# Kernel optimization log

Measured on AMD Instinct MI355X. Metric: run time of the kernel, lower is better.

## Reference

```python
import jax, jax.numpy as jnp
import numpy as np

B, T, D, V, MEM = 2, 512, 512, 256, 256


def _gru(x, h0, wih, whh, bih, bhh):
    # x: [B,T,D], h0: [B,D]; torch GRU gate order: r, z, n
    def step(h, xt):
        gi = xt @ wih.T + bih            # [B,3D]
        gh = h @ whh.T + bhh             # [B,3D]
        i_r, i_z, i_n = jnp.split(gi, 3, axis=-1)
        h_r, h_z, h_n = jnp.split(gh, 3, axis=-1)
        r = jax.nn.sigmoid(i_r + h_r)
        z = jax.nn.sigmoid(i_z + h_z)
        n = jnp.tanh(i_n + r * h_n)
        h_new = (1.0 - z) * n + z * h
        return h_new, h_new
    hT, ys = jax.lax.scan(step, h0, jnp.swapaxes(x, 0, 1))
    return jnp.swapaxes(ys, 0, 1), hT


def _layernorm(x, g, b, eps=1e-5):
    m = jnp.mean(x, axis=-1, keepdims=True)
    v = jnp.mean((x - m) ** 2, axis=-1, keepdims=True)
    return (x - m) / jnp.sqrt(v + eps) * g + b


def setup_inputs() -> dict:
    key = jax.random.key(0)
    ks = jax.random.split(key, 24)
    s = 1.0 / np.sqrt(D)
    inp = {
        'x': jax.random.randint(ks[0], (B, T), 0, V, dtype=jnp.int32),
        'h_f': jnp.zeros((1, B, D), jnp.float32),
        'h_s': jnp.zeros((1, B, D), jnp.float32),
        'soma_w': jax.random.normal(ks[1], (V, D), jnp.float32),
        'fast_wih': jax.random.normal(ks[2], (3 * D, D)) * s,
        'fast_whh': jax.random.normal(ks[3], (3 * D, D)) * s,
        'fast_bih': jax.random.normal(ks[4], (3 * D,)) * s,
        'fast_bhh': jax.random.normal(ks[5], (3 * D,)) * s,
        'slow_wih': jax.random.normal(ks[6], (3 * D, D)) * s,
        'slow_whh': jax.random.normal(ks[7], (3 * D, D)) * s,
        'slow_bih': jax.random.normal(ks[8], (3 * D,)) * s,
        'slow_bhh': jax.random.normal(ks[9], (3 * D,)) * s,
        'qkv_w': jax.random.normal(ks[10], (3 * D, D)) * s,
        'qkv_b': jax.random.normal(ks[11], (3 * D,)) * s,
        'gate_w': jax.random.normal(ks[12], (D, D)) * s,
        'gate_b': jax.random.normal(ks[13], (D,)) * s,
        'gate_g': jnp.ones((D,), jnp.float32),
        'gate_bb': jnp.zeros((D,), jnp.float32),
        'mem_bank': jax.random.normal(ks[14], (MEM, D)) * 0.1,
        'hip_qw': jax.random.normal(ks[15], (D, D)) * s,
        'hip_qb': jax.random.normal(ks[16], (D,)) * s,
        'axon_w': jax.random.normal(ks[17], (D, 4 * D)) * (0.5 * s),
        'axon_b': jax.random.normal(ks[18], (D,)) * s,
        'norm_g': jnp.ones((D,), jnp.float32),
        'norm_b': jnp.zeros((D,), jnp.float32),
    }
    return inp


def reference(x, h_f, h_s, soma_w, fast_wih, fast_whh, fast_bih, fast_bhh,
              slow_wih, slow_whh, slow_bih, slow_bhh, qkv_w, qkv_b,
              gate_w, gate_b, gate_g, gate_bb, mem_bank, hip_qw, hip_qb,
              axon_w, axon_b, norm_g, norm_b):
    d = soma_w.shape[1]
    s_in = soma_w[x]  # mod[0] == 1.0
    p_f, hf1 = _gru(s_in, h_f[0], fast_wih, fast_whh, fast_bih, fast_bhh)
    p_s, hs1 = _gru(p_f, h_s[0], slow_wih, slow_whh, slow_bih, slow_bhh)
    # LinearIntentMemory: naive cumulative outer-product linear attention
    qkv = p_s @ qkv_w.T + qkv_b
    q, k, v = jnp.split(qkv, 3, axis=-1)
    q = jax.nn.elu(q) + 1.0
    k = jax.nn.elu(k) + 1.0
    kv_cum = jnp.cumsum(jnp.einsum('bti,btj->btij', k, v), axis=1)  # [B,T,D,D]
    num = jnp.einsum('bti,btij->btj', q, kv_cum)
    den = jnp.einsum('bti,bti->bt', q, jnp.cumsum(k, axis=1))[..., None] + 1e-6
    l_mem = num / den
    # intent gate: Linear -> LayerNorm -> Tanh
    intent = jnp.tanh(_layernorm(p_s @ gate_w.T + gate_b, gate_g, gate_bb))
    # hippocampus: softmax attention over memory bank
    qh = p_s @ hip_qw.T + hip_qb
    attn = qh @ mem_bank.T / jnp.sqrt(jnp.float32(d))
    episodes = jax.nn.softmax(attn, axis=-1) @ mem_bank
    combined = jnp.concatenate([p_f, intent, l_mem, episodes], axis=-1)
    thought = _layernorm(jnp.tanh(combined @ axon_w.T + axon_b), norm_g, norm_b)
    sw = soma_w / jnp.maximum(jnp.linalg.norm(soma_w, axis=-1, keepdims=True), 1e-12)
    logits = (thought @ sw.T) * 16.0
    return (logits, thought, hf1[None], hs1[None])
```

## Files before the change

kernel.cpp:

```cpp
#include <hip/hip_runtime.h>
#include <cstddef>

#define F_ELUQK 1
#define F_CAUSAL 2
#define F_DIV 4
#define F_NN 8
#define F_SCALE 16
#define F_ROWSUM 32
#define FLAG_STRIDE 4
#define L_WGS 64
#define UNITS 8

enum : int {
  OFF_QH = 0,
  OFF_COMB = 524288,
  OFF_PS = OFF_COMB + 2097152,
  OFF_QKV = OFF_PS + 524288,
  OFF_SCORES = OFF_QKV + 1572864,
  OFF_DEN = OFF_SCORES + 524288,
  OFF_TMP = OFF_DEN + 1024,
  OFF_ATTN = OFF_TMP + 524288,
  OFF_SWN = OFF_ATTN + 262144,
  OFF_RING = OFF_SWN + 256,
  OFF_HSB = OFF_RING + 8192,
  OFF_FLAGS = OFF_HSB + 4096
};

#define BAR() __asm__ __volatile__("s_waitcnt lgkmcnt(0)\n\ts_barrier" ::: "memory")

__global__ __launch_bounds__(256) void gemm(
    const float* __restrict__ A, int lda, const float* __restrict__ B, int ldb,
    float* __restrict__ C, int ldc, int coff, int K,
    const float* __restrict__ bias, const float* __restrict__ den,
    const float* __restrict__ cscale, float* __restrict__ rsum,
    float scale, int flags, int bBatch,
    float* __restrict__ Cz, int kzoff) {
  __shared__ float As[16 * 65];
  __shared__ float Bs[16 * 65];
  int tid = threadIdx.x;
  int n0 = blockIdx.x * 64, m0 = blockIdx.y * 64;
  if (blockIdx.z) { A += kzoff; B += kzoff; C = Cz; bias = nullptr; }
  int rowoff = (m0 >> 9) * bBatch;
  int tx = tid & 15, ty = tid >> 4;

  if ((flags & F_CAUSAL) && n0 > ((m0 & 511) + 63)) {
    #pragma unroll
    for (int i = 0; i < 4; ++i)
      #pragma unroll
      for (int j = 0; j < 4; ++j)
        C[(size_t)(m0 + ty * 4 + i) * ldc + coff + n0 + tx * 4 + j] = 0.f;
    return;
  }

  float acc[4][4] = {};
  for (int k0 = 0; k0 < K; k0 += 16) {
    {
      int rr = tid >> 2, c4 = (tid & 3) << 2;
      const float* ap = A + (size_t)(m0 + rr) * lda + (k0 + c4);
      float4 av = *(const float4*)ap;
      As[(c4 + 0) * 65 + rr] = av.x;
      As[(c4 + 1) * 65 + rr] = av.y;
      As[(c4 + 2) * 65 + rr] = av.z;
      As[(c4 + 3) * 65 + rr] = av.w;
    }
    if (!(flags & F_NN)) {
      int rr = tid >> 2, c4 = (tid & 3) << 2;
      const float* bp = B + (size_t)(n0 + rr + rowoff) * ldb + (k0 + c4);
      float4 bv = *(const float4*)bp;
      Bs[(c4 + 0) * 65 + rr] = bv.x; Bs[(c4 + 1) * 65 + rr] = bv.y;
      Bs[(c4 + 2) * 65 + rr] = bv.z; Bs[(c4 + 3) * 65 + rr] = bv.w;
    } else {
      int kk = tid >> 4, n4 = (tid & 15) << 2;
      const float* bp = B + (size_t)(k0 + kk + rowoff) * ldb + (n0 + n4);
      float4 bv = *(const float4*)bp;
      Bs[kk * 65 + n4 + 0] = bv.x; Bs[kk * 65 + n4 + 1] = bv.y;
      Bs[kk * 65 + n4 + 2] = bv.z; Bs[kk * 65 + n4 + 3] = bv.w;
    }
    __syncthreads();
    #pragma unroll
    for (int k = 0; k < 16; ++k) {
      float av[4], bv[4];
      #pragma unroll
      for (int i = 0; i < 4; ++i) av[i] = As[k * 65 + ty * 4 + i];
      #pragma unroll
      for (int j = 0; j < 4; ++j) bv[j] = Bs[k * 65 + tx * 4 + j];
      #pragma unroll
      for (int i = 0; i < 4; ++i)
        #pragma unroll
        for (int j = 0; j < 4; ++j)
          acc[i][j] = fmaf(av[i], bv[j], acc[i][j]);
    }
    __syncthreads();
  }
  float rs[4] = {0.f, 0.f, 0.f, 0.f};
  #pragma unroll
  for (int i = 0; i < 4; ++i) {
    int m = m0 + ty * 4 + i;
    float dv = (flags & F_DIV) ? (1.0f / (den[m] + 1e-6f)) : 1.0f;
    #pragma unroll
    for (int j = 0; j < 4; ++j) {
      int n = n0 + tx * 4 + j;
      float v = acc[i][j];
      if (bias) v += bias[n];
      if (flags & F_ELUQK) { if (n < 1024) v = (v > 0.f) ? (v + 1.f) : __expf(v); }
      if (flags & F_CAUSAL) { if (n > (m & 511)) v = 0.f; }
      if (flags & F_SCALE) v *= scale;
      if (cscale) v *= cscale[coff + n];
      if (flags & F_DIV) v *= dv;
      C[(size_t)m * ldc + coff + n] = v;
      if (flags & F_ROWSUM) rs[i] += v;
    }
  }
  if (flags & F_ROWSUM) {
    #pragma unroll
    for (int i = 0; i < 4; ++i) {
      float s = rs[i];
      s += __shfl_xor(s, 1); s += __shfl_xor(s, 2);
      s += __shfl_xor(s, 4); s += __shfl_xor(s, 8);
      if (tx == 0) atomicAdd(rsum + (m0 + ty * 4 + i), s);
    }
  }
}

__global__ __launch_bounds__(256) void gemm3(
    const float* __restrict__ A,
    const float* __restrict__ qkvw, const float* __restrict__ qkvb,
    const float* __restrict__ gatew, const float* __restrict__ gateb,
    const float* __restrict__ hipw, const float* __restrict__ hipb,
    float* __restrict__ QKV, float* __restrict__ TMP, float* __restrict__ QH) {
  __shared__ float As[16 * 65];
  __shared__ float Bs[16 * 65];
  int tid = threadIdx.x;
  int n0 = blockIdx.x * 64, m0 = blockIdx.y * 64;
  const float* B; const float* bias; float* C; int ldc, base;
  if (n0 < 1536) { B = qkvw; bias = qkvb; C = QKV; ldc = 1536; base = 0; }
  else if (n0 < 2048) { B = gatew; bias = gateb; C = TMP; ldc = 512; base = 1536; }
  else { B = hipw; bias = hipb; C = QH; ldc = 512; base = 2048; }
  int tx = tid & 15, ty = tid >> 4;
  float acc[4][4] = {};
  for (int k0 = 0; k0 < 512; k0 += 16) {
    {
      int rr = tid >> 2, c4 = (tid & 3) << 2;
      const float* ap = A + (size_t)(m0 + rr) * 512 + (k0 + c4);
      float4 av = *(const float4*)ap;
      As[(c4 + 0) * 65 + rr] = av.x; As[(c4 + 1) * 65 + rr] = av.y;
      As[(c4 + 2) * 65 + rr] = av.z; As[(c4 + 3) * 65 + rr] = av.w;
    }
    {
      int rr = tid >> 2, c4 = (tid & 3) << 2;
      const float* bp = B + (size_t)(n0 - base + rr) * 512 + (k0 + c4);
      float4 bv = *(const float4*)bp;
      Bs[(c4 + 0) * 65 + rr] = bv.x; Bs[(c4 + 1) * 65 + rr] = bv.y;
      Bs[(c4 + 2) * 65 + rr] = bv.z; Bs[(c4 + 3) * 65 + rr] = bv.w;
    }
    __syncthreads();
    #pragma unroll
    for (int k = 0; k < 16; ++k) {
      float av[4], bv[4];
      #pragma unroll
      for (int i = 0; i < 4; ++i) av[i] = As[k * 65 + ty * 4 + i];
      #pragma unroll
      for (int j = 0; j < 4; ++j) bv[j] = Bs[k * 65 + tx * 4 + j];
      #pragma unroll
      for (int i = 0; i < 4; ++i)
        #pragma unroll
        for (int j = 0; j < 4; ++j)
          acc[i][j] = fmaf(av[i], bv[j], acc[i][j]);
    }
    __syncthreads();
  }
  #pragma unroll
  for (int i = 0; i < 4; ++i) {
    int m = m0 + ty * 4 + i;
    #pragma unroll
    for (int j = 0; j < 4; ++j) {
      int n = n0 + tx * 4 + j;
      float v = acc[i][j] + bias[n - base];
      if (n < 1024) v = (v > 0.f) ? (v + 1.f) : __expf(v);
      C[(size_t)m * ldc + (n - base)] = v;
    }
  }
}

__device__ __forceinline__ void post_flag(unsigned* flags, int w, unsigned v) {
  __hip_atomic_store(flags + (size_t)w * FLAG_STRIDE, v, __ATOMIC_RELAXED,
                     __HIP_MEMORY_SCOPE_AGENT);
}
__device__ __forceinline__ void poll64(const unsigned* flags, unsigned tgt, int lane) {
  const unsigned* p = flags + (size_t)lane * FLAG_STRIDE;
  while (__hip_atomic_load(p, __ATOMIC_RELAXED, __HIP_MEMORY_SCOPE_AGENT) < tgt)
    __builtin_amdgcn_s_sleep(1);
}
__device__ __forceinline__ void stage_pull(const unsigned long long* __restrict__ src,
                                           const unsigned* __restrict__ flags,
                                           unsigned tgt, int lane,
                                           float* __restrict__ dstLds) {
  unsigned long long v[16];
  #pragma unroll
  for (int k = 0; k < 16; ++k)
    v[k] = __hip_atomic_load(src + k * 64 + lane, __ATOMIC_RELAXED,
                             __HIP_MEMORY_SCOPE_AGENT);
  unsigned bad = 0;
  #pragma unroll
  for (int k = 0; k < 16; ++k) bad |= ((unsigned)(v[k] >> 32)) ^ tgt;
  if (!__all(bad == 0)) {
    poll64(flags, tgt, lane);
    for (;;) {
      #pragma unroll
      for (int k = 0; k < 16; ++k)
        v[k] = __hip_atomic_load(src + k * 64 + lane, __ATOMIC_RELAXED,
                                 __HIP_MEMORY_SCOPE_AGENT);
      bad = 0;
      #pragma unroll
      for (int k = 0; k < 16; ++k) bad |= ((unsigned)(v[k] >> 32)) ^ tgt;
      if (__all(bad == 0)) break;
      __builtin_amdgcn_s_sleep(1);
    }
  }
  #pragma unroll
  for (int k = 0; k < 16; ++k)
    dstLds[k * 64 + lane] = __uint_as_float((unsigned)v[k]);
}

__global__ __launch_bounds__(256, 1) void gru2_kernel(
    const float* __restrict__ soma, const int* __restrict__ x,
    const float* __restrict__ fwih, const float* __restrict__ fbih,
    const float* __restrict__ fwhh, const float* __restrict__ fbhh,
    const float* __restrict__ h0f,
    const float* __restrict__ swih, const float* __restrict__ sbih,
    const float* __restrict__ swhh, const float* __restrict__ sbhh,
    const float* __restrict__ h0s,
    float* __restrict__ pf_out,
    float* __restrict__ ps_out,
    float* __restrict__ hfT, float* __restrict__ hsT,
    unsigned long long* __restrict__ ringq,
    unsigned long long* __restrict__ hsq,
    unsigned* __restrict__ flagsA, unsigned* __restrict__ flagsB) {
  __shared__ __attribute__((aligned(16))) float hl[1024];
  __shared__ __attribute__((aligned(16))) float inb[2048];
  __shared__ float P[48];
  __shared__ float Q[48];
  __shared__ float bl[24];
  __shared__ float bi[24];
  __shared__ int xl[1024];
  int tid = threadIdx.x, wg = blockIdx.x;
  bool L1 = wg < L_WGS;
  int j0 = (wg & (L_WGS - 1)) * UNITS;
  int part = tid & 7, r = tid >> 3;
  int g = r >> 3, u = r & 7;
  int wave = tid >> 6, lane = tid & 63;
  const float* whh = L1 ? fwhh : swhh;
  const float* bhh = L1 ? fbhh : sbhh;
  const float* wih = L1 ? fwih : swih;
  const float* bih = L1 ? fbih : sbih;

  float4 wh[16], wi[16];
  if (r < 24) {
    const float* wp = whh + (size_t)(g * 512 + j0 + u) * 512 + part * 4;
    #pragma unroll
    for (int i = 0; i < 16; ++i) wh[i] = *(const float4*)(wp + i * 32);
    const float* wp2 = wih + (size_t)(g * 512 + j0 + u) * 512 + part * 4;
    #pragma unroll
    for (int i = 0; i < 16; ++i) wi[i] = *(const float4*)(wp2 + i * 32);
  }
  if (tid < 24) {
    bl[tid] = bhh[(tid >> 3) * 512 + j0 + (tid & 7)];
    bi[tid] = bih[(tid >> 3) * 512 + j0 + (tid & 7)];
  }
  if (L1) {
    for (int q = tid; q < 1024; q += 256) xl[q] = x[q];
  }
  __syncthreads();

  if (wave == 3) {
    if (L1) {
      int r0 = xl[0], r1 = xl[512];
      const float4* sp0 = (const float4*)(soma + (size_t)r0 * 512);
      const float4* sp1 = (const float4*)(soma + (size_t)r1 * 512);
      float4* dst = (float4*)inb;
      dst[lane * 2] = sp0[lane * 2]; dst[lane * 2 + 1] = sp0[lane * 2 + 1];
      dst[128 + lane * 2] = sp1[lane * 2]; dst[128 + lane * 2 + 1] = sp1[lane * 2 + 1];
    } else {
      stage_pull(ringq, flagsA, 1u, lane, inb);
    }
  }
  BAR();

  const float4* h4 = (const float4*)hl;

  if (L1) {
    for (int t = 0; t < 512; ++t) {
      float c0 = 0.f, c1 = 0.f;
      if (wave == 3) {
        if (t == 0) {
          #pragma unroll
          for (int k = 0; k < 16; ++k) hl[k * 64 + lane] = h0f[k * 64 + lane];
          int r0 = xl[1], r1 = xl[513];
          const float4* sp0 = (const float4*)(soma + (size_t)r0 * 512);
          const float4* sp1 = (const float4*)(soma + (size_t)r1 * 512);
          float4* dst = (float4*)(inb + 1024);
          dst[lane * 2] = sp0[lane * 2]; dst[lane * 2 + 1] = sp0[lane * 2 + 1];
          dst[128 + lane * 2] = sp1[lane * 2]; dst[128 + lane * 2 + 1] = sp1[lane * 2 + 1];
        } else {
          if (t + 1 < 512) {
            int r0 = xl[t + 1], r1 = xl[512 + t + 1];
            const float4* sp0 = (const float4*)(soma + (size_t)r0 * 512);
            const float4* sp1 = (const float4*)(soma + (size_t)r1 * 512);
            float4* dst = (float4*)(inb + ((t + 1) & 1) * 1024);
            dst[lane * 2] = sp0[lane * 2]; dst[lane * 2 + 1] = sp0[lane * 2 + 1];
            dst[128 + lane * 2] = sp1[lane * 2];
            dst[128 + lane * 2 + 1] = sp1[lane * 2 + 1];
            __builtin_amdgcn_sched_barrier(0);
          }
          stage_pull(ringq + (size_t)((t - 1) & 3) * 1024, flagsA,
                     (unsigned)t, lane, hl);
        }
      } else {
        const float4* f4v = (const float4*)(inb + (t & 1) * 1024);
        #pragma unroll
        for (int i = 0; i < 16; ++i) {
          float4 v = wi[i];
          float4 y0 = f4v[i * 8 + part];
          float4 y1 = f4v[128 + i * 8 + part];
          c0 += v.x * y0.x + v.y * y0.y + v.z * y0.z + v.w * y0.w;
          c1 += v.x * y1.x + v.y * y1.y + v.z * y1.z + v.w * y1.w;
        }
      }
      BAR();
      if (wave != 3) {
        float a0 = 0.f, a1 = 0.f;
        #pragma unroll
        for (int i = 0; i < 16; ++i) {
          float4 w = wh[i];
          float4 x0 = h4[i * 8 + part];
          float4 x1 = h4[128 + i * 8 + part];
          a0 += w.x * x0.x + w.y * x0.y + w.z * x0.z + w.w * x0.w;
          a1 += w.x * x1.x + w.y * x1.y + w.z * x1.z + w.w * x1.w;
        }
        a0 += __shfl_xor(a0, 1); a0 += __shfl_xor(a0, 2); a0 += __shfl_xor(a0, 4);
        a1 += __shfl_xor(a1, 1); a1 += __shfl_xor(a1, 2); a1 += __shfl_xor(a1, 4);
        c0 += __shfl_xor(c0, 1); c0 += __shfl_xor(c0, 2); c0 += __shfl_xor(c0, 4);
        c1 += __shfl_xor(c1, 1); c1 += __shfl_xor(c1, 2); c1 += __shfl_xor(c1, 4);
        if (part == 0) { P[r] = a0; P[24 + r] = a1; Q[r] = c0; Q[24 + r] = c1; }
      } else {
        if (t >= 4) poll64(flagsB, (unsigned)(t - 3), lane);
      }
      BAR();
      if (wave == 3 && lane < 16) {
        int b = lane >> 3, u2 = lane & 7, j = j0 + u2;
        float i_r = Q[b * 24 + u2] + bi[u2];
        float i_z = Q[b * 24 + 8 + u2] + bi[8 + u2];
        float i_n = Q[b * 24 + 16 + u2] + bi[16 + u2];
        float gh_r = P[b * 24 + u2] + bl[u2];
        float gh_z = P[b * 24 + 8 + u2] + bl[8 + u2];
        float gh_n = P[b * 24 + 16 + u2] + bl[16 + u2];
        float hold = hl[b * 512 + j];
        float rg = 1.0f / (1.0f + __expf(-(i_r + gh_r)));
        float zg = 1.0f / (1.0f + __expf(-(i_z + gh_z)));
        float ng = tanhf(i_n + rg * gh_n);
        float hnew = (1.0f - zg) * ng + zg * hold;
        unsigned long long pv =
            ((unsigned long long)(unsigned)(t + 1) << 32) |
            (unsigned long long)__float_as_uint(hnew);
        __hip_atomic_store(ringq + (size_t)(t & 3) * 1024 + b * 512 + j, pv,
                           __ATOMIC_RELAXED, __HIP_MEMORY_SCOPE_AGENT);
        if (lane == 0) post_flag(flagsA, wg, (unsigned)(t + 1));
        pf_out[(size_t)(b * 512 + t) * 2048 + j] = hnew;
        if (t == 511) hfT[b * 512 + j] = hnew;
      }
    }
  } else {
    for (int t2 = 0; t2 < 512; ++t2) {
      float c0 = 0.f, c1 = 0.f;
      if (wave == 3) {
        if (t2 == 0) {
          #pragma unroll
          for (int k = 0; k < 16; ++k) hl[k * 64 + lane] = h0s[k * 64 + lane];
        }
        if (t2 + 1 < 512) {
          stage_pull(ringq + (size_t)((t2 + 1) & 3) * 1024, flagsA,
                     (unsigned)(t2 + 2), lane, inb + ((t2 + 1) & 1) * 1024);
          __builtin_amdgcn_sched_barrier(0);
        }
        if (t2 > 0) {
          stage_pull(hsq + (size_t)((t2 - 1) & 1) * 1024, flagsB,
                     (unsigned)t2, lane, hl);
        }
      } else {
        const float4* f4v = (const float4*)(inb + (t2 & 1) * 1024);
        #pragma unroll
        for (int i = 0; i < 16; ++i) {
          float4 v = wi[i];
          float4 y0 = f4v[i * 8 + part];
          float4 y1 = f4v[128 + i * 8 + part];
          c0 += v.x * y0.x + v.y * y0.y + v.z * y0.z + v.w * y0.w;
          c1 += v.x * y1.x + v.y * y1.y + v.z * y1.z + v.w * y1.w;
        }
      }
      BAR();
      if (wave != 3) {
        float a0 = 0.f, a1 = 0.f;
        #pragma unroll
        for (int i = 0; i < 16; ++i) {
          float4 w = wh[i];
          float4 x0 = h4[i * 8 + part];
          float4 x1 = h4[128 + i * 8 + part];
          a0 += w.x * x0.x + w.y * x0.y + w.z * x0.z + w.w * x0.w;
          a1 += w.x * x1.x + w.y * x1.y + w.z * x1.z + w.w * x1.w;
        }
        a0 += __shfl_xor(a0, 1); a0 += __shfl_xor(a0, 2); a0 += __shfl_xor(a0, 4);
        a1 += __shfl_xor(a1, 1); a1 += __shfl_xor(a1, 2); a1 += __shfl_xor(a1, 4);
        c0 += __shfl_xor(c0, 1); c0 += __shfl_xor(c0, 2); c0 += __shfl_xor(c0, 4);
        c1 += __shfl_xor(c1, 1); c1 += __shfl_xor(c1, 2); c1 += __shfl_xor(c1, 4);
        if (part == 0) { P[r] = a0; P[24 + r] = a1; Q[r] = c0; Q[24 + r] = c1; }
      }
      BAR();
      if (wave == 3 && lane < 16) {
        int b = lane >> 3, u2 = lane & 7, j = j0 + u2;
        float i_r = Q[b * 24 + u2] + bi[u2];
        float i_z = Q[b * 24 + 8 + u2] + bi[8 + u2];
        float i_n = Q[b * 24 + 16 + u2] + bi[16 + u2];
        float gh_r = P[b * 24 + u2] + bl[u2];
        float gh_z = P[b * 24 + 8 + u2] + bl[8 + u2];
        float gh_n = P[b * 24 + 16 + u2] + bl[16 + u2];
        float hold = hl[b * 512 + j];
        float rg = 1.0f / (1.0f + __expf(-(i_r + gh_r)));
        float zg = 1.0f / (1.0f + __expf(-(i_z + gh_z)));
        float ng = tanhf(i_n + rg * gh_n);
        float hnew = (1.0f - zg) * ng + zg * hold;
        unsigned long long pv =
            ((unsigned long long)(unsigned)(t2 + 1) << 32) |
            (unsigned long long)__float_as_uint(hnew);
        __hip_atomic_store(hsq + (size_t)(t2 & 1) * 1024 + b * 512 + j, pv,
                           __ATOMIC_RELAXED, __HIP_MEMORY_SCOPE_AGENT);
        if (lane == 0) post_flag(flagsB, wg - L_WGS, (unsigned)(t2 + 1));
        ps_out[(size_t)(b * 512 + t2) * 512 + j] = hnew;
        if (t2 == 511) hsT[b * 512 + j] = hnew;
      }
    }
  }
}

__global__ __launch_bounds__(256) void softmax_kernel(float* __restrict__ a) {
  int m = blockIdx.x, tid = threadIdx.x;
  float v = a[(size_t)m * 256 + tid];
  float mx = v;
  #pragma unroll
  for (int off = 32; off > 0; off >>= 1) mx = fmaxf(mx, __shfl_down(mx, off));
  __shared__ float r4[4];
  __shared__ float s4[4];
  if ((tid & 63) == 0) r4[tid >> 6] = mx;
  __syncthreads();
  mx = fmaxf(fmaxf(r4[0], r4[1]), fmaxf(r4[2], r4[3]));
  float e = __expf(v - mx);
  float s = e;
  #pragma unroll
  for (int off = 32; off > 0; off >>= 1) s += __shfl_down(s, off);
  if ((tid & 63) == 0) s4[tid >> 6] = s;
  __syncthreads();
  s = s4[0] + s4[1] + s4[2] + s4[3];
  a[(size_t)m * 256 + tid] = e / s;
}

__global__ __launch_bounds__(256) void ln_kernel(
    const float* __restrict__ src, const float* __restrict__ src2,
    float* __restrict__ dst, int ldd, int dcoff,
    const float* __restrict__ gv, const float* __restrict__ bv, int tanhFirst) {
  int m = blockIdx.x, tid = threadIdx.x;
  float x0 = src[(size_t)m * 512 + tid];
  float x1 = src[(size_t)m * 512 + 256 + tid];
  if (src2) { x0 += src2[(size_t)m * 512 + tid]; x1 += src2[(size_t)m * 512 + 256 + tid]; }
  if (tanhFirst) { x0 = tanhf(x0); x1 = tanhf(x1); }
  float s = x0 + x1, ss = x0 * x0 + x1 * x1;
  #pragma unroll
  for (int off = 32; off > 0; off >>= 1) { s += __shfl_down(s, off); ss += __shfl_down(ss, off); }
  __shared__ float rs[4], rss[4];
  if ((tid & 63) == 0) { rs[tid >> 6] = s; rss[tid >> 6] = ss; }
  __syncthreads();
  float st = rs[0] + rs[1] + rs[2] + rs[3];
  float sst = rss[0] + rss[1] + rss[2] + rss[3];
  float mean = st * (1.0f / 512.0f);
  float var = sst * (1.0f / 512.0f) - mean * mean;
  float inv = rsqrtf(var + 1e-5f);
  float y0 = (x0 - mean) * inv * gv[tid] + bv[tid];
  float y1 = (x1 - mean) * inv * gv[256 + tid] + bv[256 + tid];
  if (!tanhFirst) { y0 = tanhf(y0); y1 = tanhf(y1); }
  dst[(size_t)m * ldd + dcoff + tid] = y0;
  dst[(size_t)m * ldd + dcoff + 256 + tid] = y1;
}

__global__ __launch_bounds__(256) void swinv_kernel(const float* __restrict__ soma,
                                                    float* __restrict__ swn) {
  int r = blockIdx.x, tid = threadIdx.x;
  float x0 = soma[(size_t)r * 512 + tid];
  float x1 = soma[(size_t)r * 512 + 256 + tid];
  float ss = x0 * x0 + x1 * x1;
  #pragma unroll
  for (int off = 32; off > 0; off >>= 1) ss += __shfl_down(ss, off);
  __shared__ float r4[4];
  if ((tid & 63) == 0) r4[tid >> 6] = ss;
  __syncthreads();
  if (tid == 0) {
    float norm = fmaxf(sqrtf(r4[0] + r4[1] + r4[2] + r4[3]), 1e-12f);
    swn[r] = 16.0f / norm;
  }
}

extern "C" void kernel_launch(void* const* d_in, const int* in_sizes, int n_in,
                              void* d_out, int out_size, void* d_ws, size_t ws_size,
                              hipStream_t stream) {
  (void)in_sizes; (void)n_in; (void)out_size; (void)ws_size;
  float* W = (float*)d_ws;
  float* outf = (float*)d_out;
  const int* x = (const int*)d_in[0];
  const float* soma = (const float*)d_in[3];

  hipMemsetAsync((char*)d_ws + (size_t)OFF_RING * 4, 0, 51200, stream);
  hipMemsetAsync((char*)d_ws + (size_t)OFF_DEN * 4, 0, 4096, stream);

  gru2_kernel<<<2 * L_WGS, 256, 0, stream>>>(soma, x,
      (const float*)d_in[4], (const float*)d_in[6],
      (const float*)d_in[5], (const float*)d_in[7], (const float*)d_in[1],
      (const float*)d_in[8], (const float*)d_in[10],
      (const float*)d_in[9], (const float*)d_in[11], (const float*)d_in[2],
      W + OFF_COMB, W + OFF_PS, outf + 786432, outf + 787456,
      (unsigned long long*)(W + OFF_RING), (unsigned long long*)(W + OFF_HSB),
      (unsigned*)(W + OFF_FLAGS),
      (unsigned*)(W + OFF_FLAGS) + L_WGS * FLAG_STRIDE);

  gemm3<<<dim3(40, 16), 256, 0, stream>>>(W + OFF_PS,
      (const float*)d_in[12], (const float*)d_in[13],
      (const float*)d_in[14], (const float*)d_in[15],
      (const float*)d_in[19], (const float*)d_in[20],
      W + OFF_QKV, W + OFF_TMP, W + OFF_QH);

  gemm<<<dim3(8, 16), 256, 0, stream>>>(W + OFF_QKV, 1536, W + OFF_QKV + 512, 1536,
      W + OFF_SCORES, 512, 0, 512, nullptr, nullptr, nullptr, W + OFF_DEN,
      1.f, F_CAUSAL | F_ROWSUM, 512, nullptr, 0);

  gemm<<<dim3(8, 16), 256, 0, stream>>>(W + OFF_SCORES, 512, W + OFF_QKV + 1024, 1536,
      W + OFF_COMB, 2048, 1024, 512, nullptr, W + OFF_DEN, nullptr, nullptr,
      1.f, F_NN | F_DIV, 512, nullptr, 0);

  ln_kernel<<<1024, 256, 0, stream>>>(W + OFF_TMP, nullptr, W + OFF_COMB, 2048, 512,
      (const float*)d_in[16], (const float*)d_in[17], 0);

  gemm<<<dim3(4, 16), 256, 0, stream>>>(W + OFF_QH, 512, (const float*)d_in[18], 512,
      W + OFF_ATTN, 256, 0, 512, nullptr, nullptr, nullptr, nullptr,
      0.04419417382415922f, F_SCALE, 0, nullptr, 0);
  softmax_kernel<<<1024, 256, 0, stream>>>(W + OFF_ATTN);
  gemm<<<dim3(8, 16), 256, 0, stream>>>(W + OFF_ATTN, 256, (const float*)d_in[18], 512,
      W + OFF_COMB, 2048, 1536, 256, nullptr, nullptr, nullptr, nullptr,
      1.f, F_NN, 0, nullptr, 0);

  gemm<<<dim3(8, 16, 2), 256, 0, stream>>>(W + OFF_COMB, 2048, (const float*)d_in[21], 2048,
      W + OFF_TMP, 512, 0, 1024, (const float*)d_in[22], nullptr, nullptr, nullptr,
      1.f, 0, 0, W + OFF_QH, 1024);

  ln_kernel<<<1024, 256, 0, stream>>>(W + OFF_TMP, W + OFF_QH, outf + 262144, 512, 0,
      (const float*)d_in[23], (const float*)d_in[24], 1);

  swinv_kernel<<<256, 256, 0, stream>>>(soma, W + OFF_SWN);
  gemm<<<dim3(4, 16), 256, 0, stream>>>(outf + 262144, 512, soma, 512,
      outf, 256, 0, 512, nullptr, nullptr, W + OFF_SWN, nullptr,
      1.f, 0, 0, nullptr, 0);
}
```

Measured before the change: 1.739 ms.

## Precompute fast-GRU input projection in helper workgroups inside the GRU kernel

Adds 64 extra workgroups to the persistent GRU kernel that compute the fast layer's input projection (embedding gather times W_ih) as a tiled GEMM into the QKV scratch buffer. They publish per-chunk completion counters that the recurrent workgroups poll. The fast-layer recurrent workgroups drop their per-step embedding gather and input matvec and instead read the precomputed gate inputs, shortening each serial step. Risks include extra workgroups competing for CUs and polling latency on the chunk counters; the scratch buffer is reused later by the QKV GEMM.

```diff
diff --git a/kernel.cpp b/kernel.cpp
--- a/kernel.cpp
+++ b/kernel.cpp
@@ -23,7 +23,8 @@
   OFF_SWN = OFF_ATTN + 262144,
   OFF_RING = OFF_SWN + 256,
   OFF_HSB = OFF_RING + 8192,
-  OFF_FLAGS = OFF_HSB + 4096
+  OFF_FLAGS = OFF_HSB + 4096,
+  OFF_GIC = OFF_FLAGS + 512
 };
 
 #define BAR() __asm__ __volatile__("s_waitcnt lgkmcnt(0)\n\ts_barrier" ::: "memory")
@@ -191,6 +192,25 @@
   while (__hip_atomic_load(p, __ATOMIC_RELAXED, __HIP_MEMORY_SCOPE_AGENT) < tgt)
     __builtin_amdgcn_s_sleep(1);
 }
+__device__ __forceinline__ void tagload16(const unsigned long long* __restrict__ src,
+                                          unsigned expect, int lane,
+                                          float* __restrict__ dstLds) {
+  unsigned long long v[16];
+  for (;;) {
+    #pragma unroll
+    for (int k = 0; k < 16; ++k)
+      v[k] = __hip_atomic_load(src + k * 64 + lane, __ATOMIC_RELAXED,
+                               __HIP_MEMORY_SCOPE_AGENT);
+    unsigned bad = 0;
+    #pragma unroll
+    for (int k = 0; k < 16; ++k) bad |= ((unsigned)(v[k] >> 32)) ^ expect;
+    if (__all(bad == 0)) break;
+    __builtin_amdgcn_s_sleep(1);
+  }
+  #pragma unroll
+  for (int k = 0; k < 16; ++k)
+    dstLds[k * 64 + lane] = __uint_as_float((unsigned)v[k]);
+}
 __device__ __forceinline__ void stage_pull(const unsigned long long* __restrict__ src,
                                            const unsigned* __restrict__ flags,
                                            unsigned tgt, int lane,
@@ -235,15 +255,74 @@
     float* __restrict__ hfT, float* __restrict__ hsT,
     unsigned long long* __restrict__ ringq,
     unsigned long long* __restrict__ hsq,
-    unsigned* __restrict__ flagsA, unsigned* __restrict__ flagsB) {
+    unsigned* __restrict__ flagsA, unsigned* __restrict__ flagsB,
+    float* __restrict__ gi,
+    unsigned* __restrict__ gic) {
   __shared__ __attribute__((aligned(16))) float hl[1024];
   __shared__ __attribute__((aligned(16))) float inb[2048];
   __shared__ float P[48];
   __shared__ float Q[48];
   __shared__ float bl[24];
   __shared__ float bi[24];
-  __shared__ int xl[1024];
+  __shared__ float As2[16 * 65];
+  __shared__ float Bs2[16 * 65];
+  __shared__ int xs[64];
   int tid = threadIdx.x, wg = blockIdx.x;
+
+  if (wg >= 2 * L_WGS) {
+    int gw = wg - 2 * L_WGS;
+    int tx = tid & 15, ty = tid >> 4;
+    for (int g = gw; g < 384; g += 64) {
+      int c = g / 24, ct = g - c * 24;
+      int cbase = c * 32, n0 = ct * 64;
+      if (tid < 64) xs[tid] = x[cbase + (tid & 31) + ((tid >> 5) << 9)];
+      __syncthreads();
+      float acc[4][4] = {};
+      for (int k0 = 0; k0 < 512; k0 += 16) {
+        {
+          int rr = tid >> 2, c4 = (tid & 3) << 2;
+          const float* ap = soma + (size_t)xs[rr] * 512 + (k0 + c4);
+          float4 av = *(const float4*)ap;
+          As2[(c4 + 0) * 65 + rr] = av.x; As2[(c4 + 1) * 65 + rr] = av.y;
+          As2[(c4 + 2) * 65 + rr] = av.z; As2[(c4 + 3) * 65 + rr] = av.w;
+          const float* bp = fwih + (size_t)(n0 + rr) * 512 + (k0 + c4);
+          float4 bv = *(const float4*)bp;
+          Bs2[(c4 + 0) * 65 + rr] = bv.x; Bs2[(c4 + 1) * 65 + rr] = bv.y;
+          Bs2[(c4 + 2) * 65 + rr] = bv.z; Bs2[(c4 + 3) * 65 + rr] = bv.w;
+        }
+        __syncthreads();
+        #pragma unroll
+        for (int k = 0; k < 16; ++k) {
+          float av[4], bv[4];
+          #pragma unroll
+          for (int i = 0; i < 4; ++i) av[i] = As2[k * 65 + ty * 4 + i];
+          #pragma unroll
+          for (int j = 0; j < 4; ++j) bv[j] = Bs2[k * 65 + tx * 4 + j];
+          #pragma unroll
+          for (int i = 0; i < 4; ++i)
+            #pragma unroll
+            for (int j = 0; j < 4; ++j)
+              acc[i][j] = fmaf(av[i], bv[j], acc[i][j]);
+        }
+        __syncthreads();
+      }
+      #pragma unroll
+      for (int i = 0; i < 4; ++i) {
+        int rr = ty * 4 + i;
+        int m = cbase + (rr & 31) + ((rr >> 5) << 9);
+        #pragma unroll
+        for (int j = 0; j < 4; ++j)
+          gi[(size_t)m * 1536 + n0 + tx * 4 + j] = acc[i][j];
+      }
+      __threadfence();
+      __syncthreads();
+      if (tid == 0)
+        __hip_atomic_fetch_add(gic + c, 1u, __ATOMIC_RELEASE,
+                               __HIP_MEMORY_SCOPE_AGENT);
+    }
+    return;
+  }
+
   bool L1 = wg < L_WGS;
   int j0 = (wg & (L_WGS - 1)) * UNITS;
   int part = tid & 7, r = tid >> 3;
@@ -251,38 +330,27 @@
   int wave = tid >> 6, lane = tid & 63;
   const float* whh = L1 ? fwhh : swhh;
   const float* bhh = L1 ? fbhh : sbhh;
-  const float* wih = L1 ? fwih : swih;
-  const float* bih = L1 ? fbih : sbih;
+  const float* bihp = L1 ? fbih : sbih;
 
   float4 wh[16], wi[16];
   if (r < 24) {
     const float* wp = whh + (size_t)(g * 512 + j0 + u) * 512 + part * 4;
     #pragma unroll
     for (int i = 0; i < 16; ++i) wh[i] = *(const float4*)(wp + i * 32);
-    const float* wp2 = wih + (size_t)(g * 512 + j0 + u) * 512 + part * 4;
-    #pragma unroll
-    for (int i = 0; i < 16; ++i) wi[i] = *(const float4*)(wp2 + i * 32);
+    if (!L1) {
+      const float* wp2 = swih + (size_t)(g * 512 + j0 + u) * 512 + part * 4;
+      #pragma unroll
+      for (int i = 0; i < 16; ++i) wi[i] = *(const float4*)(wp2 + i * 32);
+    }
   }
   if (tid < 24) {
     bl[tid] = bhh[(tid >> 3) * 512 + j0 + (tid & 7)];
-    bi[tid] = bih[(tid >> 3) * 512 + j0 + (tid & 7)];
-  }
-  if (L1) {
-    for (int q = tid; q < 1024; q += 256) xl[q] = x[q];
+    bi[tid] = bihp[(tid >> 3) * 512 + j0 + (tid & 7)];
   }
   __syncthreads();
 
-  if (wave == 3) {
-    if (L1) {
-      int r0 = xl[0], r1 = xl[512];
-      const float4* sp0 = (const float4*)(soma + (size_t)r0 * 512);
-      const float4* sp1 = (const float4*)(soma + (size_t)r1 * 512);
-      float4* dst = (float4*)inb;
-      dst[lane * 2] = sp0[lane * 2]; dst[lane * 2 + 1] = sp0[lane * 2 + 1];
-      dst[128 + lane * 2] = sp1[lane * 2]; dst[128 + lane * 2 + 1] = sp1[lane * 2 + 1];
-    } else {
-      stage_pull(ringq, flagsA, 1u, lane, inb);
-    }
+  if (!L1 && wave == 3) {
+    stage_pull(ringq, flagsA, 1u, lane, inb);
   }
   BAR();
 
@@ -290,40 +358,25 @@
 
   if (L1) {
     for (int t = 0; t < 512; ++t) {
-      float c0 = 0.f, c1 = 0.f;
+      float gi_r = 0.f, gi_z = 0.f, gi_n = 0.f;
       if (wave == 3) {
+        if ((t & 31) == 0) {
+          const unsigned* gc = gic + (t >> 5);
+          while (__hip_atomic_load(gc, __ATOMIC_ACQUIRE,
+                                   __HIP_MEMORY_SCOPE_AGENT) < 24u)
+            __builtin_amdgcn_s_sleep(1);
+        }
+        if (lane < 16) {
+          const float* gp = gi + (size_t)((lane >> 3) * 512 + t) * 1536
+                              + j0 + (lane & 7);
+          gi_r = gp[0]; gi_z = gp[512]; gi_n = gp[1024];
+        }
         if (t == 0) {
           #pragma unroll
           for (int k = 0; k < 16; ++k) hl[k * 64 + lane] = h0f[k * 64 + lane];
-          int r0 = xl[1], r1 = xl[513];
-          const float4* sp0 = (const float4*)(soma + (size_t)r0 * 512);
-          const float4* sp1 = (const float4*)(soma + (size_t)r1 * 512);
-          float4* dst = (float4*)(inb + 1024);
-          dst[lane * 2] = sp0[lane * 2]; dst[lane * 2 + 1] = sp0[lane * 2 + 1];
-          dst[128 + lane * 2] = sp1[lane * 2]; dst[128 + lane * 2 + 1] = sp1[lane * 2 + 1];
         } else {
-          if (t + 1 < 512) {
-            int r0 = xl[t + 1], r1 = xl[512 + t + 1];
-            const float4* sp0 = (const float4*)(soma + (size_t)r0 * 512);
-            const float4* sp1 = (const float4*)(soma + (size_t)r1 * 512);
-            float4* dst = (float4*)(inb + ((t + 1) & 1) * 1024);
-            dst[lane * 2] = sp0[lane * 2]; dst[lane * 2 + 1] = sp0[lane * 2 + 1];
-            dst[128 + lane * 2] = sp1[lane * 2];
-            dst[128 + lane * 2 + 1] = sp1[lane * 2 + 1];
-            __builtin_amdgcn_sched_barrier(0);
-          }
-          stage_pull(ringq + (size_t)((t - 1) & 3) * 1024, flagsA,
-                     (unsigned)t, lane, hl);
-        }
-      } else {
-        const float4* f4v = (const float4*)(inb + (t & 1) * 1024);
-        #pragma unroll
-        for (int i = 0; i < 16; ++i) {
-          float4 v = wi[i];
-          float4 y0 = f4v[i * 8 + part];
-          float4 y1 = f4v[128 + i * 8 + part];
-          c0 += v.x * y0.x + v.y * y0.y + v.z * y0.z + v.w * y0.w;
-          c1 += v.x * y1.x + v.y * y1.y + v.z * y1.z + v.w * y1.w;
+          poll64(flagsA, (unsigned)t, lane);
+          tagload16(ringq + (size_t)((t - 1) & 3) * 1024, (unsigned)t, lane, hl);
         }
       }
       BAR();
@@ -339,18 +392,16 @@
         }
         a0 += __shfl_xor(a0, 1); a0 += __shfl_xor(a0, 2); a0 += __shfl_xor(a0, 4);
         a1 += __shfl_xor(a1, 1); a1 += __shfl_xor(a1, 2); a1 += __shfl_xor(a1, 4);
-        c0 += __shfl_xor(c0, 1); c0 += __shfl_xor(c0, 2); c0 += __shfl_xor(c0, 4);
-        c1 += __shfl_xor(c1, 1); c1 += __shfl_xor(c1, 2); c1 += __shfl_xor(c1, 4);
-        if (part == 0) { P[r] = a0; P[24 + r] = a1; Q[r] = c0; Q[24 + r] = c1; }
+        if (part == 0 && r < 24) { P[r] = a0; P[24 + r] = a1; }
       } else {
         if (t >= 4) poll64(flagsB, (unsigned)(t - 3), lane);
       }
       BAR();
       if (wave == 3 && lane < 16) {
         int b = lane >> 3, u2 = lane & 7, j = j0 + u2;
-        float i_r = Q[b * 24 + u2] + bi[u2];
-        float i_z = Q[b * 24 + 8 + u2] + bi[8 + u2];
-        float i_n = Q[b * 24 + 16 + u2] + bi[16 + u2];
+        float i_r = gi_r + bi[u2];
+        float i_z = gi_z + bi[8 + u2];
+        float i_n = gi_n + bi[16 + u2];
         float gh_r = P[b * 24 + u2] + bl[u2];
         float gh_z = P[b * 24 + 8 + u2] + bl[8 + u2];
         float gh_n = P[b * 24 + 16 + u2] + bl[16 + u2];
@@ -412,7 +463,7 @@
         a1 += __shfl_xor(a1, 1); a1 += __shfl_xor(a1, 2); a1 += __shfl_xor(a1, 4);
         c0 += __shfl_xor(c0, 1); c0 += __shfl_xor(c0, 2); c0 += __shfl_xor(c0, 4);
         c1 += __shfl_xor(c1, 1); c1 += __shfl_xor(c1, 2); c1 += __shfl_xor(c1, 4);
-        if (part == 0) { P[r] = a0; P[24 + r] = a1; Q[r] = c0; Q[24 + r] = c1; }
+        if (part == 0 && r < 24) { P[r] = a0; P[24 + r] = a1; Q[r] = c0; Q[24 + r] = c1; }
       }
       BAR();
       if (wave == 3 && lane < 16) {
@@ -515,10 +566,10 @@
   const int* x = (const int*)d_in[0];
   const float* soma = (const float*)d_in[3];
 
-  hipMemsetAsync((char*)d_ws + (size_t)OFF_RING * 4, 0, 51200, stream);
+  hipMemsetAsync((char*)d_ws + (size_t)OFF_RING * 4, 0, 51264, stream);
   hipMemsetAsync((char*)d_ws + (size_t)OFF_DEN * 4, 0, 4096, stream);
 
-  gru2_kernel<<<2 * L_WGS, 256, 0, stream>>>(soma, x,
+  gru2_kernel<<<3 * L_WGS, 256, 0, stream>>>(soma, x,
       (const float*)d_in[4], (const float*)d_in[6],
       (const float*)d_in[5], (const float*)d_in[7], (const float*)d_in[1],
       (const float*)d_in[8], (const float*)d_in[10],
@@ -526,7 +577,8 @@
       W + OFF_COMB, W + OFF_PS, outf + 786432, outf + 787456,
       (unsigned long long*)(W + OFF_RING), (unsigned long long*)(W + OFF_HSB),
       (unsigned*)(W + OFF_FLAGS),
-      (unsigned*)(W + OFF_FLAGS) + L_WGS * FLAG_STRIDE);
+      (unsigned*)(W + OFF_FLAGS) + L_WGS * FLAG_STRIDE,
+      W + OFF_QKV, (unsigned*)(W + OFF_GIC));
 
   gemm3<<<dim3(40, 16), 256, 0, stream>>>(W + OFF_PS,
       (const float*)d_in[12], (const float*)d_in[13],
```

Measured after the change: 1.905 ms. +9.5%, slower.
